# Kernel optimization log

Measured on AMD Instinct MI355X. Metric: run time of the kernel, lower is better.

Reference implementation:

```python
import jax, jax.numpy as jnp
import numpy as np

N_NODES = 100000
N_EDGES = 3200000
IN_FEATS = 512
HIDDEN = 16
NUM_CLASSES = 40


def setup_inputs() -> dict:
    key = jax.random.key(0)
    k1, k2, k3, k4, k5, k6 = jax.random.split(key, 6)
    x = jax.random.normal(k1, (N_NODES, IN_FEATS), dtype=jnp.float32)
    edge_index = jax.random.randint(k2, (2, N_EDGES), 0, N_NODES, dtype=jnp.int64)
    # Glorot-ish init for GCN weights
    W1 = jax.random.normal(k3, (IN_FEATS, HIDDEN), dtype=jnp.float32) / np.sqrt(IN_FEATS)
    b1 = jnp.zeros((HIDDEN,), dtype=jnp.float32)
    W2 = jax.random.normal(k4, (HIDDEN, NUM_CLASSES), dtype=jnp.float32) / np.sqrt(HIDDEN)
    b2 = jnp.zeros((NUM_CLASSES,), dtype=jnp.float32)
    return {"x": x, "edge_index": edge_index, "W1": W1, "b1": b1, "W2": W2, "b2": b2}


def _gcn_norm(edge_index, num_nodes):
    # Add self-loops (PyG GCNConv default), then symmetric normalization
    loops = jnp.arange(num_nodes, dtype=edge_index.dtype)
    src = jnp.concatenate([edge_index[0], loops])
    dst = jnp.concatenate([edge_index[1], loops])
    deg = jax.ops.segment_sum(jnp.ones_like(dst, dtype=jnp.float32), dst,
                              num_segments=num_nodes)
    dinv = jnp.where(deg > 0, jax.lax.rsqrt(deg), 0.0)
    norm = dinv[src] * dinv[dst]  # [E + N]
    return src, dst, norm


def _gcn_conv(x, W, b, src, dst, norm, num_nodes):
    h = x @ W                                   # transform first: [N, d_out]
    msg = h[src] * norm[:, None]                # gather + scale: [E+N, d_out]
    agg = jax.ops.segment_sum(msg, dst, num_segments=num_nodes)
    return agg + b


def reference(x, edge_index, W1, b1, W2, b2):
    num_nodes = x.shape[0]
    src, dst, norm = _gcn_norm(edge_index, num_nodes)
    h = _gcn_conv(x, W1, b1, src, dst, norm, num_nodes)
    h = jax.nn.relu(h)
    # F.dropout(training=self.training): eval mode -> identity (deterministic reference)
    h = _gcn_conv(h, W2, b2, src, dst, norm, num_nodes)
    return jax.nn.log_softmax(h, axis=1)
```

## Files before the change

### kernel.cpp

```cpp
#include <hip/hip_runtime.h>
#include <hip/hip_bf16.h>
#include <math.h>

#define N_NODES 100000
#define N_EDGES 3200000
#define IN_F    512
#define HID     16
#define NCLS    40
#define NB      512
#define NPB     196
#define CAPW    8192
#define NBLK    1024
#define EPB     3125
#define EPT     13

typedef unsigned short ushort_t;
struct ushort4_t { ushort_t x, y, z, w; };

__device__ __forceinline__ float bf16_to_f32(ushort_t u) {
    unsigned int b = ((unsigned int)u) << 16;
    return __uint_as_float(b);
}
__device__ __forceinline__ ushort_t f32_to_bf16(float f) {
    __hip_bfloat16 h = __float2bfloat16(f);
    return *(ushort_t*)&h;
}

__device__ __forceinline__ int load_edge(const void* ei, int is64, int idx) {
    if (is64) return (int)((const long long*)ei)[idx];
    return ((const int*)ei)[idx];
}

__global__ __launch_bounds__(256) void kPre(const int* __restrict__ ei,
                                            int* __restrict__ flag,
                                            int* __restrict__ gcur) {
    int i = blockIdx.x * 256 + threadIdx.x;
    if (i < NB) gcur[i] = i * CAPW;
    if (blockIdx.x == 0) {
        __shared__ int s_nz;
        if (threadIdx.x == 0) s_nz = 0;
        __syncthreads();
        int nz = 0;
        for (int k = threadIdx.x; k < 1024; k += 256)
            if (ei[2 * k + 1] != 0) nz = 1;
        if (nz) atomicOr(&s_nz, 1);
        __syncthreads();
        if (threadIdx.x == 0) flag[0] = s_nz ? 0 : 1;
    }
}

__global__ __launch_bounds__(256) void kB(const void* __restrict__ ei,
                                          const int* __restrict__ flag,
                                          int* __restrict__ gcur,
                                          int* __restrict__ binned) {
    __shared__ int hist[NB];
    __shared__ int base[NB];
    int tid = threadIdx.x;
    for (int i = tid; i < NB; i += 256) hist[i] = 0;
    __syncthreads();
    int is64 = flag[0];
    int off0 = blockIdx.x * EPB;
    int dreg[EPT];
#pragma unroll
    for (int u = 0; u < EPT; ++u) {
        int i = u * 256 + tid;
        if (i < EPB) {
            int d = load_edge(ei, is64, N_EDGES + off0 + i);
            dreg[u] = d;
            atomicAdd(&hist[d / NPB], 1);
        } else {
            dreg[u] = -1;
        }
    }
    __syncthreads();
    for (int i = tid; i < NB; i += 256) {
        int c = hist[i];
        base[i] = c ? atomicAdd(&gcur[i], c) : 0;
        hist[i] = 0;
    }
    __syncthreads();
#pragma unroll
    for (int u = 0; u < EPT; ++u) {
        int i = u * 256 + tid;
        if (i < EPB) {
            int s = load_edge(ei, is64, off0 + i);
            int d = dreg[u];
            int b = d / NPB;
            int o = atomicAdd(&hist[b], 1);
            binned[base[b] + o] = (s << 8) | (d - b * NPB);
        }
    }
}

__global__ __launch_bounds__(256) void kSort(const int* __restrict__ gcur,
                                             int* __restrict__ binned,
                                             int* __restrict__ nstart,
                                             int* __restrict__ bend,
                                             float* __restrict__ dinv) {
    __shared__ int elist[CAPW];
    __shared__ int ih[NPB];
    __shared__ int lscan[NPB + 1];
    int b = blockIdx.x, tid = threadIdx.x;
    int beg = b * CAPW;
    int cnt = gcur[b] - beg;
    if (cnt > CAPW) cnt = CAPW;
    if (cnt < 0) cnt = 0;
    if (tid < NPB) ih[tid] = 0;
    __syncthreads();
    for (int k = tid; k < cnt; k += 256) {
        int p = binned[beg + k];
        elist[k] = p;
        atomicAdd(&ih[p & 255], 1);
    }
    __syncthreads();
    if (tid == 0) {
        int run = 0;
        for (int i = 0; i < NPB; ++i) { lscan[i] = run; run += ih[i]; }
        lscan[NPB] = run;
        bend[b] = beg + run;
    }
    __syncthreads();
    if (tid < NPB) {
        int n = b * NPB + tid;
        if (n < N_NODES) dinv[n] = rsqrtf((float)(ih[tid] + 1));
        nstart[n] = beg + lscan[tid];
        ih[tid] = lscan[tid];
    }
    __syncthreads();
    for (int k = tid; k < cnt; k += 256) {
        int p = elist[k];
        int pos = atomicAdd(&ih[p & 255], 1);
        binned[beg + pos] = p >> 8;
    }
}

__global__ __launch_bounds__(128) void k_gemm1(const float* __restrict__ x,
                                               const float* __restrict__ W1,
                                               const float* __restrict__ dinv,
                                               ushort_t* __restrict__ hsb) {
    __shared__ float Ws[IN_F * HID];
    for (int i = threadIdx.x; i < IN_F * HID; i += 128) Ws[i] = W1[i];
    __syncthreads();
    int n = blockIdx.x * 128 + threadIdx.x;
    if (n >= N_NODES) return;
    float acc[HID];
#pragma unroll
    for (int j = 0; j < HID; ++j) acc[j] = 0.0f;
    const float4* xr = (const float4*)(x + (size_t)n * IN_F);
    for (int k16 = 0; k16 < IN_F / 16; ++k16) {
        float4 xv[4];
#pragma unroll
        for (int q = 0; q < 4; ++q) xv[q] = xr[k16 * 4 + q];
#pragma unroll
        for (int q = 0; q < 4; ++q) {
            int kb = (k16 * 4 + q) * 4;
#pragma unroll
            for (int i = 0; i < 4; ++i) {
                float xs = (&xv[q].x)[i];
                const float4* wr = (const float4*)(Ws + (kb + i) * HID);
#pragma unroll
                for (int j4 = 0; j4 < 4; ++j4) {
                    float4 w = wr[j4];
                    acc[j4 * 4 + 0] += xs * w.x;
                    acc[j4 * 4 + 1] += xs * w.y;
                    acc[j4 * 4 + 2] += xs * w.z;
                    acc[j4 * 4 + 3] += xs * w.w;
                }
            }
        }
    }
    float di = dinv[n];
    ushort_t* hn = hsb + (size_t)n * HID;
#pragma unroll
    for (int j = 0; j < HID; ++j) hn[j] = f32_to_bf16(acc[j] * di);
}

__device__ __forceinline__ void gather_sum4(const int* __restrict__ sorted,
                                            int beg, int end,
                                            const ushort_t* __restrict__ feat,
                                            int esub, int f4,
                                            float* __restrict__ r) {
    float ax = 0.0f, ay = 0.0f, az = 0.0f, aw = 0.0f;
    int k = beg;
    if (k + 16 <= end) {
        int s[4];
#pragma unroll
        for (int u = 0; u < 4; ++u) s[u] = sorted[k + 4 * u + esub];
        for (; k + 32 <= end; k += 16) {
            int s2[4];
#pragma unroll
            for (int u = 0; u < 4; ++u) s2[u] = sorted[k + 16 + 4 * u + esub];
#pragma unroll
            for (int u = 0; u < 4; ++u) {
                ushort4_t v = *(const ushort4_t*)&feat[(size_t)s[u] * HID + 4 * f4];
                ax += bf16_to_f32(v.x); ay += bf16_to_f32(v.y);
                az += bf16_to_f32(v.z); aw += bf16_to_f32(v.w);
            }
#pragma unroll
            for (int u = 0; u < 4; ++u) s[u] = s2[u];
        }
#pragma unroll
        for (int u = 0; u < 4; ++u) {
            ushort4_t v = *(const ushort4_t*)&feat[(size_t)s[u] * HID + 4 * f4];
            ax += bf16_to_f32(v.x); ay += bf16_to_f32(v.y);
            az += bf16_to_f32(v.z); aw += bf16_to_f32(v.w);
        }
        k += 16;
    }
    for (; k + 4 <= end; k += 4) {
        int s = sorted[k + esub];
        ushort4_t v = *(const ushort4_t*)&feat[(size_t)s * HID + 4 * f4];
        ax += bf16_to_f32(v.x); ay += bf16_to_f32(v.y);
        az += bf16_to_f32(v.z); aw += bf16_to_f32(v.w);
    }
    if (k + esub < end) {
        int s = sorted[k + esub];
        ushort4_t v = *(const ushort4_t*)&feat[(size_t)s * HID + 4 * f4];
        ax += bf16_to_f32(v.x); ay += bf16_to_f32(v.y);
        az += bf16_to_f32(v.z); aw += bf16_to_f32(v.w);
    }
#pragma unroll
    for (int m = 4; m <= 8; m <<= 1) {
        ax += __shfl_xor(ax, m, 16);
        ay += __shfl_xor(ay, m, 16);
        az += __shfl_xor(az, m, 16);
        aw += __shfl_xor(aw, m, 16);
    }
    r[0] = ax; r[1] = ay; r[2] = az; r[3] = aw;
}

__global__ __launch_bounds__(256) void kAgg1(const int* __restrict__ nstart,
                                             const int* __restrict__ bend,
                                             const int* __restrict__ sorted,
                                             const ushort_t* __restrict__ hsb,
                                             const float* __restrict__ dinv,
                                             const float* __restrict__ b1,
                                             ushort_t* __restrict__ h1sb) {
    int tid = threadIdx.x;
    int g = tid >> 4, lane = tid & 15;
    int esub = lane >> 2, f4 = lane & 3;
    int n = blockIdx.x * 16 + g;
    int b = n / NPB, il = n - b * NPB;
    int beg = nstart[n];
    int end = (il == NPB - 1) ? bend[b] : nstart[n + 1];
    float r[4];
    gather_sum4(sorted, beg, end, hsb, esub, f4, r);
    if (esub == 0) {
        float di = dinv[n];
        ushort4_t sv = *(const ushort4_t*)&hsb[(size_t)n * HID + 4 * f4];
        float s0 = bf16_to_f32(sv.x), s1 = bf16_to_f32(sv.y);
        float s2 = bf16_to_f32(sv.z), s3 = bf16_to_f32(sv.w);
        const float* bp = b1 + 4 * f4;
        ushort4_t o;
        o.x = f32_to_bf16(fmaxf(di * (r[0] + s0) + bp[0], 0.0f) * di);
        o.y = f32_to_bf16(fmaxf(di * (r[1] + s1) + bp[1], 0.0f) * di);
        o.z = f32_to_bf16(fmaxf(di * (r[2] + s2) + bp[2], 0.0f) * di);
        o.w = f32_to_bf16(fmaxf(di * (r[3] + s3) + bp[3], 0.0f) * di);
        *(ushort4_t*)&h1sb[(size_t)n * HID + 4 * f4] = o;
    }
}

__global__ __launch_bounds__(256) void kAggOut(const int* __restrict__ nstart,
                                               const int* __restrict__ bend,
                                               const int* __restrict__ sorted,
                                               const ushort_t* __restrict__ h1sb,
                                               const float* __restrict__ dinv,
                                               const float* __restrict__ W2,
                                               const float* __restrict__ b2,
                                               float* __restrict__ out) {
    __shared__ float a2[16][HID + 1];
    __shared__ float Ws[HID * NCLS];
    __shared__ float bs[NCLS];
    int tid = threadIdx.x;
    for (int i = tid; i < HID * NCLS; i += 256) Ws[i] = W2[i];
    for (int i = tid; i < NCLS; i += 256) bs[i] = b2[i];

    int g = tid >> 4, lane = tid & 15;
    int esub = lane >> 2, f4 = lane & 3;
    int n = blockIdx.x * 16 + g;
    int b = n / NPB, il = n - b * NPB;
    int beg = nstart[n];
    int end = (il == NPB - 1) ? bend[b] : nstart[n + 1];
    float r[4];
    gather_sum4(sorted, beg, end, h1sb, esub, f4, r);
    if (esub == 0) {
        float di = dinv[n];
        ushort4_t sv = *(const ushort4_t*)&h1sb[(size_t)n * HID + 4 * f4];
        a2[g][4 * f4 + 0] = di * (r[0] + bf16_to_f32(sv.x));
        a2[g][4 * f4 + 1] = di * (r[1] + bf16_to_f32(sv.y));
        a2[g][4 * f4 + 2] = di * (r[2] + bf16_to_f32(sv.z));
        a2[g][4 * f4 + 3] = di * (r[3] + bf16_to_f32(sv.w));
    }
    __syncthreads();

    float l0 = bs[lane], l1 = bs[lane + 16];
    float l2 = (lane < 8) ? bs[lane + 32] : -1e30f;
#pragma unroll
    for (int j = 0; j < HID; ++j) {
        float av = a2[g][j];
        const float* wr = Ws + j * NCLS;
        l0 += av * wr[lane];
        l1 += av * wr[lane + 16];
        if (lane < 8) l2 += av * wr[lane + 32];
    }
    float m = fmaxf(l0, fmaxf(l1, l2));
#pragma unroll
    for (int off = 8; off >= 1; off >>= 1)
        m = fmaxf(m, __shfl_xor(m, off, 16));
    float e = expf(l0 - m) + expf(l1 - m) + ((lane < 8) ? expf(l2 - m) : 0.0f);
#pragma unroll
    for (int off = 8; off >= 1; off >>= 1)
        e += __shfl_xor(e, off, 16);
    float lse = m + logf(e);
    float* on = out + (size_t)n * NCLS;
    on[lane] = l0 - lse;
    on[lane + 16] = l1 - lse;
    if (lane < 8) on[lane + 32] = l2 - lse;
}

extern "C" void kernel_launch(void* const* d_in, const int* in_sizes, int n_in,
                              void* d_out, int out_size, void* d_ws, size_t ws_size,
                              hipStream_t stream) {
    const float* x  = (const float*)d_in[0];
    const void*  ei = d_in[1];
    const float* W1 = (const float*)d_in[2];
    const float* b1 = (const float*)d_in[3];
    const float* W2 = (const float*)d_in[4];
    const float* b2 = (const float*)d_in[5];
    float* out = (float*)d_out;

    int*      iws    = (int*)d_ws;
    float*    fws    = (float*)d_ws;
    int*      gcur   = iws;
    int*      bend   = iws + 2048;
    int*      flag   = iws + 4096;
    float*    dinv   = fws + 8192;
    int*      nstart = iws + 108192;
    ushort_t* hsb    = (ushort_t*)(iws + 212992);
    ushort_t* h1sb   = (ushort_t*)(iws + 1012992);
    int*      binned = iws + 1812992;

    const int B = 256;

    kPre<<<(NB + B - 1) / B, B, 0, stream>>>((const int*)ei, flag, gcur);
    kB<<<NBLK, B, 0, stream>>>(ei, flag, gcur, binned);
    kSort<<<NB, B, 0, stream>>>(gcur, binned, nstart, bend, dinv);
    k_gemm1<<<(N_NODES + 127) / 128, 128, 0, stream>>>(x, W1, dinv, hsb);
    kAgg1<<<N_NODES / 16, B, 0, stream>>>(nstart, bend, binned, hsb, dinv, b1, h1sb);
    kAggOut<<<N_NODES / 16, B, 0, stream>>>(nstart, bend, binned, h1sb, dinv, W2, b2, out);
}
```

Measured before the change: 206.8 us.

## Stage per-bin edge lists in LDS and process half-bins per block

Aggregation kernels now launch one block per half bin, cooperatively load the bin's node offsets and sorted source indices into shared memory, then loop over nodes reading indices from LDS. This aims to coalesce index loads and cut per-node global offset reads. In exchange it launches far fewer blocks, adds block-wide syncs per iteration in the output kernel, drops the index prefetch in the gather loop, and silently truncates edges if a half-bin exceeds SCAP.

```diff
diff --git a/kernel.cpp b/kernel.cpp
--- a/kernel.cpp
+++ b/kernel.cpp
@@ -9,7 +9,9 @@
 #define NCLS    40
 #define NB      512
 #define NPB     196
+#define HNPB    98
 #define CAPW    8192
+#define SCAP    4608
 #define NBLK    1024
 #define EPB     3125
 #define EPT     13
@@ -175,46 +177,35 @@
     for (int j = 0; j < HID; ++j) hn[j] = f32_to_bf16(acc[j] * di);
 }
 
-__device__ __forceinline__ void gather_sum4(const int* __restrict__ sorted,
-                                            int beg, int end,
-                                            const ushort_t* __restrict__ feat,
-                                            int esub, int f4,
-                                            float* __restrict__ r) {
+__device__ __forceinline__ void gather_sum4_lds(const int* __restrict__ elist,
+                                                int kb, int ke,
+                                                const ushort_t* __restrict__ feat,
+                                                int esub, int f4,
+                                                float* __restrict__ r) {
     float ax = 0.0f, ay = 0.0f, az = 0.0f, aw = 0.0f;
-    int k = beg;
-    if (k + 16 <= end) {
+    int k = kb;
+    for (; k + 16 <= ke; k += 16) {
         int s[4];
 #pragma unroll
-        for (int u = 0; u < 4; ++u) s[u] = sorted[k + 4 * u + esub];
-        for (; k + 32 <= end; k += 16) {
-            int s2[4];
-#pragma unroll
-            for (int u = 0; u < 4; ++u) s2[u] = sorted[k + 16 + 4 * u + esub];
-#pragma unroll
-            for (int u = 0; u < 4; ++u) {
-                ushort4_t v = *(const ushort4_t*)&feat[(size_t)s[u] * HID + 4 * f4];
-                ax += bf16_to_f32(v.x); ay += bf16_to_f32(v.y);
-                az += bf16_to_f32(v.z); aw += bf16_to_f32(v.w);
-            }
-#pragma unroll
-            for (int u = 0; u < 4; ++u) s[u] = s2[u];
-        }
+        for (int u = 0; u < 4; ++u) s[u] = elist[k + 4 * u + esub];
+        ushort4_t v[4];
+#pragma unroll
+        for (int u = 0; u < 4; ++u)
+            v[u] = *(const ushort4_t*)&feat[(size_t)s[u] * HID + 4 * f4];
 #pragma unroll
         for (int u = 0; u < 4; ++u) {
-            ushort4_t v = *(const ushort4_t*)&feat[(size_t)s[u] * HID + 4 * f4];
-            ax += bf16_to_f32(v.x); ay += bf16_to_f32(v.y);
-            az += bf16_to_f32(v.z); aw += bf16_to_f32(v.w);
-        }
-        k += 16;
-    }
-    for (; k + 4 <= end; k += 4) {
-        int s = sorted[k + esub];
+            ax += bf16_to_f32(v[u].x); ay += bf16_to_f32(v[u].y);
+            az += bf16_to_f32(v[u].z); aw += bf16_to_f32(v[u].w);
+        }
+    }
+    for (; k + 4 <= ke; k += 4) {
+        int s = elist[k + esub];
         ushort4_t v = *(const ushort4_t*)&feat[(size_t)s * HID + 4 * f4];
         ax += bf16_to_f32(v.x); ay += bf16_to_f32(v.y);
         az += bf16_to_f32(v.z); aw += bf16_to_f32(v.w);
     }
-    if (k + esub < end) {
-        int s = sorted[k + esub];
+    if (k + esub < ke) {
+        int s = elist[k + esub];
         ushort4_t v = *(const ushort4_t*)&feat[(size_t)s * HID + 4 * f4];
         ax += bf16_to_f32(v.x); ay += bf16_to_f32(v.y);
         az += bf16_to_f32(v.z); aw += bf16_to_f32(v.w);
@@ -236,27 +227,42 @@
                                              const float* __restrict__ dinv,
                                              const float* __restrict__ b1,
                                              ushort_t* __restrict__ h1sb) {
+    __shared__ int elist[SCAP];
+    __shared__ int offs[NPB + 1];
     int tid = threadIdx.x;
+    int b = blockIdx.x >> 1, h = blockIdx.x & 1;
+    int beg_w = b * CAPW;
+    for (int i = tid; i <= NPB; i += 256)
+        offs[i] = ((i < NPB) ? nstart[b * NPB + i] : bend[b]) - beg_w;
+    __syncthreads();
+    int k0 = offs[h * HNPB];
+    int k1 = offs[h * HNPB + HNPB];
+    int sl = k1 - k0;
+    if (sl > SCAP) sl = SCAP;
+    for (int k = tid; k < sl; k += 256) elist[k] = sorted[beg_w + k0 + k];
+    __syncthreads();
+
     int g = tid >> 4, lane = tid & 15;
     int esub = lane >> 2, f4 = lane & 3;
-    int n = blockIdx.x * 16 + g;
-    int b = n / NPB, il = n - b * NPB;
-    int beg = nstart[n];
-    int end = (il == NPB - 1) ? bend[b] : nstart[n + 1];
-    float r[4];
-    gather_sum4(sorted, beg, end, hsb, esub, f4, r);
-    if (esub == 0) {
-        float di = dinv[n];
-        ushort4_t sv = *(const ushort4_t*)&hsb[(size_t)n * HID + 4 * f4];
-        float s0 = bf16_to_f32(sv.x), s1 = bf16_to_f32(sv.y);
-        float s2 = bf16_to_f32(sv.z), s3 = bf16_to_f32(sv.w);
-        const float* bp = b1 + 4 * f4;
-        ushort4_t o;
-        o.x = f32_to_bf16(fmaxf(di * (r[0] + s0) + bp[0], 0.0f) * di);
-        o.y = f32_to_bf16(fmaxf(di * (r[1] + s1) + bp[1], 0.0f) * di);
-        o.z = f32_to_bf16(fmaxf(di * (r[2] + s2) + bp[2], 0.0f) * di);
-        o.w = f32_to_bf16(fmaxf(di * (r[3] + s3) + bp[3], 0.0f) * di);
-        *(ushort4_t*)&h1sb[(size_t)n * HID + 4 * f4] = o;
+    for (int il = h * HNPB + g; il < h * HNPB + HNPB; il += 16) {
+        int n = b * NPB + il;
+        if (n >= N_NODES) continue;
+        int kb = offs[il] - k0;
+        int ke = offs[il + 1] - k0;
+        if (ke > sl) ke = sl;
+        float r[4];
+        gather_sum4_lds(elist, kb, ke, hsb, esub, f4, r);
+        if (esub == 0) {
+            float di = dinv[n];
+            ushort4_t sv = *(const ushort4_t*)&hsb[(size_t)n * HID + 4 * f4];
+            const float* bp = b1 + 4 * f4;
+            ushort4_t o;
+            o.x = f32_to_bf16(fmaxf(di * (r[0] + bf16_to_f32(sv.x)) + bp[0], 0.0f) * di);
+            o.y = f32_to_bf16(fmaxf(di * (r[1] + bf16_to_f32(sv.y)) + bp[1], 0.0f) * di);
+            o.z = f32_to_bf16(fmaxf(di * (r[2] + bf16_to_f32(sv.z)) + bp[2], 0.0f) * di);
+            o.w = f32_to_bf16(fmaxf(di * (r[3] + bf16_to_f32(sv.w)) + bp[3], 0.0f) * di);
+            *(ushort4_t*)&h1sb[(size_t)n * HID + 4 * f4] = o;
+        }
     }
 }
 
@@ -268,54 +274,77 @@
                                                const float* __restrict__ W2,
                                                const float* __restrict__ b2,
                                                float* __restrict__ out) {
+    __shared__ int elist[SCAP];
+    __shared__ int offs[NPB + 1];
     __shared__ float a2[16][HID + 1];
     __shared__ float Ws[HID * NCLS];
     __shared__ float bs[NCLS];
     int tid = threadIdx.x;
+    int b = blockIdx.x >> 1, h = blockIdx.x & 1;
+    int beg_w = b * CAPW;
     for (int i = tid; i < HID * NCLS; i += 256) Ws[i] = W2[i];
     for (int i = tid; i < NCLS; i += 256) bs[i] = b2[i];
+    for (int i = tid; i <= NPB; i += 256)
+        offs[i] = ((i < NPB) ? nstart[b * NPB + i] : bend[b]) - beg_w;
+    __syncthreads();
+    int k0 = offs[h * HNPB];
+    int k1 = offs[h * HNPB + HNPB];
+    int sl = k1 - k0;
+    if (sl > SCAP) sl = SCAP;
+    for (int k = tid; k < sl; k += 256) elist[k] = sorted[beg_w + k0 + k];
+    __syncthreads();
 
     int g = tid >> 4, lane = tid & 15;
     int esub = lane >> 2, f4 = lane & 3;
-    int n = blockIdx.x * 16 + g;
-    int b = n / NPB, il = n - b * NPB;
-    int beg = nstart[n];
-    int end = (il == NPB - 1) ? bend[b] : nstart[n + 1];
-    float r[4];
-    gather_sum4(sorted, beg, end, h1sb, esub, f4, r);
-    if (esub == 0) {
-        float di = dinv[n];
-        ushort4_t sv = *(const ushort4_t*)&h1sb[(size_t)n * HID + 4 * f4];
-        a2[g][4 * f4 + 0] = di * (r[0] + bf16_to_f32(sv.x));
-        a2[g][4 * f4 + 1] = di * (r[1] + bf16_to_f32(sv.y));
-        a2[g][4 * f4 + 2] = di * (r[2] + bf16_to_f32(sv.z));
-        a2[g][4 * f4 + 3] = di * (r[3] + bf16_to_f32(sv.w));
-    }
-    __syncthreads();
-
-    float l0 = bs[lane], l1 = bs[lane + 16];
-    float l2 = (lane < 8) ? bs[lane + 32] : -1e30f;
-#pragma unroll
-    for (int j = 0; j < HID; ++j) {
-        float av = a2[g][j];
-        const float* wr = Ws + j * NCLS;
-        l0 += av * wr[lane];
-        l1 += av * wr[lane + 16];
-        if (lane < 8) l2 += av * wr[lane + 32];
-    }
-    float m = fmaxf(l0, fmaxf(l1, l2));
-#pragma unroll
-    for (int off = 8; off >= 1; off >>= 1)
-        m = fmaxf(m, __shfl_xor(m, off, 16));
-    float e = expf(l0 - m) + expf(l1 - m) + ((lane < 8) ? expf(l2 - m) : 0.0f);
-#pragma unroll
-    for (int off = 8; off >= 1; off >>= 1)
-        e += __shfl_xor(e, off, 16);
-    float lse = m + logf(e);
-    float* on = out + (size_t)n * NCLS;
-    on[lane] = l0 - lse;
-    on[lane + 16] = l1 - lse;
-    if (lane < 8) on[lane + 32] = l2 - lse;
+    const int NIT = (HNPB + 15) / 16;
+    for (int it = 0; it < NIT; ++it) {
+        int il = h * HNPB + it * 16 + g;
+        int n = b * NPB + il;
+        bool valid = (il < h * HNPB + HNPB) && (n < N_NODES);
+        if (valid) {
+            int kb = offs[il] - k0;
+            int ke = offs[il + 1] - k0;
+            if (ke > sl) ke = sl;
+            float r[4];
+            gather_sum4_lds(elist, kb, ke, h1sb, esub, f4, r);
+            if (esub == 0) {
+                float di = dinv[n];
+                ushort4_t sv = *(const ushort4_t*)&h1sb[(size_t)n * HID + 4 * f4];
+                a2[g][4 * f4 + 0] = di * (r[0] + bf16_to_f32(sv.x));
+                a2[g][4 * f4 + 1] = di * (r[1] + bf16_to_f32(sv.y));
+                a2[g][4 * f4 + 2] = di * (r[2] + bf16_to_f32(sv.z));
+                a2[g][4 * f4 + 3] = di * (r[3] + bf16_to_f32(sv.w));
+            }
+        }
+        __syncthreads();
+        if (valid) {
+            float l0 = bs[lane], l1 = bs[lane + 16];
+            float l2 = (lane < 8) ? bs[lane + 32] : -1e30f;
+#pragma unroll
+            for (int j = 0; j < HID; ++j) {
+                float av = a2[g][j];
+                const float* wr = Ws + j * NCLS;
+                l0 += av * wr[lane];
+                l1 += av * wr[lane + 16];
+                if (lane < 8) l2 += av * wr[lane + 32];
+            }
+            float m = fmaxf(l0, fmaxf(l1, l2));
+#pragma unroll
+            for (int off = 8; off >= 1; off >>= 1)
+                m = fmaxf(m, __shfl_xor(m, off, 16));
+            float e = expf(l0 - m) + expf(l1 - m) +
+                      ((lane < 8) ? expf(l2 - m) : 0.0f);
+#pragma unroll
+            for (int off = 8; off >= 1; off >>= 1)
+                e += __shfl_xor(e, off, 16);
+            float lse = m + logf(e);
+            float* on = out + (size_t)n * NCLS;
+            on[lane] = l0 - lse;
+            on[lane + 16] = l1 - lse;
+            if (lane < 8) on[lane + 32] = l2 - lse;
+        }
+        __syncthreads();
+    }
 }
 
 extern "C" void kernel_launch(void* const* d_in, const int* in_sizes, int n_in,
@@ -346,6 +375,6 @@
     kB<<<NBLK, B, 0, stream>>>(ei, flag, gcur, binned);
     kSort<<<NB, B, 0, stream>>>(gcur, binned, nstart, bend, dinv);
     k_gemm1<<<(N_NODES + 127) / 128, 128, 0, stream>>>(x, W1, dinv, hsb);
-    kAgg1<<<N_NODES / 16, B, 0, stream>>>(nstart, bend, binned, hsb, dinv, b1, h1sb);
-    kAggOut<<<N_NODES / 16, B, 0, stream>>>(nstart, bend, binned, h1sb, dinv, W2, b2, out);
-}
+    kAgg1<<<NB * 2, B, 0, stream>>>(nstart, bend, binned, hsb, dinv, b1, h1sb);
+    kAggOut<<<NB * 2, B, 0, stream>>>(nstart, bend, binned, h1sb, dinv, W2, b2, out);
+}
```

Measured after the change: 213.9 us. 3.5% more time.
